# Kernel tuning notes

Hardware: AMD Instinct MI355X
Metric: run time of the kernel (lower is better)

The kernel has to match this reference:

```python
import jax, jax.numpy as jnp
import numpy as np

N_HEAD = 8
D_HEAD = 64  # emb_size == d_model // n_head


def _proj(x, w):
    # x: (B, 1, d_model, max_len), w: (n_head*emb_size, 1, 25, 1) -> conv VALID
    y = jax.lax.conv_general_dilated(
        x, w, window_strides=(1, 1), padding='VALID',
        dimension_numbers=('NCHW', 'OIHW', 'NCHW'))  # (B, C, H1, L)
    B, C, H1, L = y.shape
    y = y.reshape(B, C, H1 // N_HEAD, N_HEAD, L).mean(axis=3)  # (B, C, H2, L)
    # view(B, -1, n_head, d_head).transpose(1, 2) -> (B, n_head, S, d_head)
    y = y.reshape(B, -1, N_HEAD, D_HEAD).transpose(0, 2, 1, 3)
    return y


def setup_inputs() -> dict:
    key = jax.random.key(0)
    ks = jax.random.split(key, 7)
    B, d_model, max_len = 8, 512, 16
    C = N_HEAD * D_HEAD  # 512
    return {
        'query': jax.random.normal(ks[0], (B, 1, d_model, max_len), jnp.float32),
        'key':   jax.random.normal(ks[1], (B, 1, d_model, max_len), jnp.float32),
        'value': jax.random.normal(ks[2], (B, 1, d_model, max_len), jnp.float32),
        'wq': jax.random.normal(ks[3], (C, 1, 25, 1), jnp.float32) * 0.1,
        'wk': jax.random.normal(ks[4], (C, 1, 25, 1), jnp.float32) * 0.1,
        'wv': jax.random.normal(ks[5], (C, 1, 25, 1), jnp.float32) * 0.1,
        'w_out': jax.random.normal(ks[6], (1, 1, 1, 1), jnp.float32),
        'b_out': jnp.zeros((1,), jnp.float32),
    }


def reference(query, key, value, wq, wk, wv, w_out, b_out):
    q = _proj(query, wq)   # (B, H, S, Dh)
    k = _proj(key, wk)
    v = _proj(value, wv)
    scale = 1.0 / jnp.sqrt(jnp.asarray(D_HEAD, q.dtype))
    scores = jnp.einsum('bhqd,bhkd->bhqk', q, k) * scale
    attn = jax.nn.softmax(scores, axis=-1)  # dropout is identity in eval
    x = jnp.einsum('bhqk,bhkd->bhqd', attn, v)
    B = x.shape[0]
    x = x.transpose(0, 2, 1, 3).reshape(B, -1, N_HEAD * D_HEAD)  # (B, S, d_model)
    # conv_out: 1x1 Conv2d(1,1) == scalar scale + bias
    x = x * w_out.reshape(()) + b_out.reshape(())
    return x, attn
```

## Files before the change

### kernel.cpp

```cpp
#include <hip/hip_runtime.h>
#include <hip/hip_bf16.h>
#include <cstdint>
#include <cstddef>

#define B_    8
#define H_    8
#define BH_   64
#define S_    976
#define SP_   992
#define D_    64
#define DM_   512
#define L_    16
#define H2_   61
#define KW_   25
#define EFF_  32
#define XOFF  3997696
#define NWB   49152
#define OSTR  68

typedef __attribute__((ext_vector_type(8))) short bf16x8;
typedef __attribute__((ext_vector_type(4))) float f32x4;

__device__ __forceinline__ unsigned short f2bfu(float f) {
    union { float f; unsigned u; } v; v.f = f;
    unsigned u = v.u;
    u += 0x7fffu + ((u >> 16) & 1u);
    return (unsigned short)(u >> 16);
}
__device__ __forceinline__ unsigned packbf(float a, float b) {
    return (unsigned)f2bfu(a) | ((unsigned)f2bfu(b) << 16);
}
__device__ __forceinline__ float bflo(unsigned u) {
    union { unsigned u; float f; } v; v.u = u << 16; return v.f;
}
__device__ __forceinline__ float bfhi(unsigned u) {
    union { unsigned u; float f; } v; v.u = u & 0xffff0000u; return v.f;
}

__global__ __launch_bounds__(256) void wbar_kernel(
    const float* __restrict__ wq, const float* __restrict__ wk,
    const float* __restrict__ wv, float* __restrict__ wbar,
    short* __restrict__ vtws) {
    int idx = blockIdx.x * 256 + threadIdx.x;
    if (idx < NWB) {
        int t  = idx & 31;
        int c  = (idx >> 5) & 511;
        int tz = idx >> 14;
        const float* w = (tz == 0) ? wq : (tz == 1) ? wk : wv;
        int jlo = (t - 24 > 0) ? t - 24 : 0;
        int jhi = (t < 7) ? t : 7;
        float s = 0.f;
        for (int j = jlo; j <= jhi; ++j) s += w[c * KW_ + (t - j)];
        wbar[idx] = s * 0.125f;
    } else {
        int p = idx - NWB;
        int bh = p >> 10;
        int dh = (p >> 4) & 63;
        int s  = S_ + (p & 15);
        vtws[((size_t)bh * D_ + dh) * SP_ + s] = 0;
    }
}

__global__ __launch_bounds__(256) void proj_kernel(
    const float* __restrict__ qin, const float* __restrict__ kin,
    const float* __restrict__ vin, const float* __restrict__ wbar,
    short* __restrict__ qws, short* __restrict__ kws, short* __restrict__ vtws) {
    __shared__ float xl[536 * L_];
    int blk = blockIdx.x;
    int cg  = blk & 15;
    int b   = (blk >> 4) & 7;
    int tz  = blk >> 7;
    const float* x = (tz == 0) ? qin : (tz == 1) ? kin : vin;

    const float4* xb4 = (const float4*)(x + b * DM_ * L_);
    float4* xl4 = (float4*)xl;
    for (int i = threadIdx.x; i < DM_ * L_ / 4; i += 256) xl4[i] = xb4[i];
    for (int i = DM_ * L_ + threadIdx.x; i < 536 * L_; i += 256) xl[i] = 0.f;

    int c_local = threadIdx.x >> 3;
    int plane   = threadIdx.x & 7;
    int c       = cg * 32 + c_local;
    float wreg[EFF_];
    const float4* wb4 = (const float4*)(wbar + ((size_t)tz * DM_ + c) * EFF_);
    #pragma unroll
    for (int i = 0; i < 8; ++i) {
        float4 t4 = wb4[i];
        wreg[4*i+0] = t4.x; wreg[4*i+1] = t4.y;
        wreg[4*i+2] = t4.z; wreg[4*i+3] = t4.w;
    }
    __syncthreads();

    for (int m = 0; m < 32; ++m) {
        int pg  = plane + 8 * m;
        int h2b = pg >> 4;
        int l   = pg & 15;
        float acc[4] = {0.f, 0.f, 0.f, 0.f};
        #pragma unroll
        for (int k = 0; k < 56; ++k) {
            float xv = xl[(h2b * 32 + k) * L_ + l];
            #pragma unroll
            for (int d = 0; d < 4; ++d) {
                int t = k - 8 * d;
                if (t >= 0 && t < EFF_) acc[d] = fmaf(xv, wreg[t], acc[d]);
            }
        }
        #pragma unroll
        for (int d = 0; d < 4; ++d) {
            int h2 = h2b * 4 + d;
            if (h2 < H2_) {
                int f    = c * S_ + h2 * L_ + l;
                int s    = f >> 9;
                int head = (f >> 6) & 7;
                int dh   = f & 63;
                int bh   = b * H_ + head;
                short bv = (short)f2bfu(acc[d]);
                if (tz == 0)      qws[((size_t)bh * S_ + s) * D_ + dh] = bv;
                else if (tz == 1) kws[((size_t)bh * S_ + s) * D_ + dh] = bv;
                else              vtws[((size_t)bh * D_ + dh) * SP_ + s] = bv;
            }
        }
    }
}

__global__ __launch_bounds__(256) void attn_kernel(
    const short* __restrict__ qws, const short* __restrict__ kws,
    const short* __restrict__ vtws, const float* __restrict__ w_out,
    const float* __restrict__ b_out, float* __restrict__ out) {
    __shared__ short plds[4][16 * 40];
    __shared__ float olds[2][16 * OSTR];
    __shared__ float sums[2][2][16];

    int w    = threadIdx.x >> 6;
    int lane = threadIdx.x & 63;
    int l16  = lane & 15;
    int g    = lane >> 4;
    int p    = w >> 1;
    int h    = w & 1;

    int blk = blockIdx.x;
    int xcd = blk & 7;
    int j   = blk >> 3;
    int bh  = xcd + 8 * (j / 31);
    int pr  = j % 31;
    int qt  = pr * 2 + p;
    bool valid = qt < H2_;
    int s0 = qt * 16;

    int t0 = h ? 30 : 0;
    int nt = h ? 31 : 30;

    unsigned pp[31][2];
    float inv = 0.f;

    if (valid) {
        const short* qb = qws + ((size_t)bh * S_ + s0 + l16) * D_ + g * 8;
        bf16x8 q0 = *(const bf16x8*)qb;
        bf16x8 q1 = *(const bf16x8*)(qb + 32);
        const short* kb0 = kws + ((size_t)bh * S_ + t0 * 16 + l16) * D_ + g * 8;

        float sa = 0.f, sb = 0.f, sc_ = 0.f, sd = 0.f;
        #pragma unroll
        for (int ct = 0; ct < 31; ++ct) {
            if (ct < nt) {
                const short* kb = kb0 + (size_t)ct * 16 * D_;
                bf16x8 k0 = *(const bf16x8*)kb;
                bf16x8 k1 = *(const bf16x8*)(kb + 32);
                f32x4 acc = {0.f, 0.f, 0.f, 0.f};
                acc = __builtin_amdgcn_mfma_f32_16x16x32_bf16(k0, q0, acc, 0, 0, 0);
                acc = __builtin_amdgcn_mfma_f32_16x16x32_bf16(k1, q1, acc, 0, 0, 0);
                float e0 = __expf(acc[0] * 0.125f);
                float e1 = __expf(acc[1] * 0.125f);
                float e2 = __expf(acc[2] * 0.125f);
                float e3 = __expf(acc[3] * 0.125f);
                sa += e0; sb += e1; sc_ += e2; sd += e3;
                pp[ct][0] = packbf(e0, e1);
                pp[ct][1] = packbf(e2, e3);
            }
        }
        float sum = (sa + sb) + (sc_ + sd);
        sum += __shfl_xor(sum, 16);
        sum += __shfl_xor(sum, 32);
        if (lane < 16) sums[p][h][l16] = sum;
    }
    __syncthreads();
    if (valid) inv = 1.f / (sums[p][0][l16] + sums[p][1][l16]);

    f32x4 o0 = {0.f,0.f,0.f,0.f}, o1 = {0.f,0.f,0.f,0.f};
    f32x4 o2 = {0.f,0.f,0.f,0.f}, o3 = {0.f,0.f,0.f,0.f};

    if (valid) {
        float* arow = out + XOFF + ((size_t)bh * S_ + s0 + l16) * S_;
        short* pl = &plds[w][0];
        const short* vrow = vtws + ((size_t)bh * D_ + l16) * SP_ + g * 8;

        #pragma unroll
        for (int c = 0; c < 15; ++c) {
            #pragma unroll
            for (int t = 0; t < 2; ++t) {
                int lt = 2 * c + t;
                int gt = t0 + lt;
                unsigned u0 = pp[lt][0], u1 = pp[lt][1];
                f32x4 pv = { bflo(u0) * inv, bfhi(u0) * inv,
                             bflo(u1) * inv, bfhi(u1) * inv };
                __builtin_nontemporal_store(pv, (f32x4*)(arow + gt * 16 + g * 4));
                uint2 upk = {u0, u1};
                *(uint2*)(void*)(pl + l16 * 40 + t * 16 + g * 4) = upk;
            }
            __threadfence_block();
            bf16x8 pa = *(const bf16x8*)(pl + l16 * 40 + g * 8);
            const short* vb = vrow + t0 * 16 + c * 32;
            o0 = __builtin_amdgcn_mfma_f32_16x16x32_bf16(pa, *(const bf16x8*)(vb), o0, 0, 0, 0);
            o1 = __builtin_amdgcn_mfma_f32_16x16x32_bf16(pa, *(const bf16x8*)(vb + 16 * SP_), o1, 0, 0, 0);
            o2 = __builtin_amdgcn_mfma_f32_16x16x32_bf16(pa, *(const bf16x8*)(vb + 32 * SP_), o2, 0, 0, 0);
            o3 = __builtin_amdgcn_mfma_f32_16x16x32_bf16(pa, *(const bf16x8*)(vb + 48 * SP_), o3, 0, 0, 0);
        }

        if (h) {
            unsigned u0 = pp[30][0], u1 = pp[30][1];
            f32x4 pv = { bflo(u0) * inv, bfhi(u0) * inv,
                         bflo(u1) * inv, bfhi(u1) * inv };
            __builtin_nontemporal_store(pv, (f32x4*)(arow + 60 * 16 + g * 4));
            uint2 upk = {u0, u1};
            *(uint2*)(void*)(pl + l16 * 40 + g * 4) = upk;
            uint2 zz = {0u, 0u};
            *(uint2*)(void*)(pl + l16 * 40 + 16 + g * 4) = zz;
            __threadfence_block();
            bf16x8 pa = *(const bf16x8*)(pl + l16 * 40 + g * 8);
            const short* vb = vrow + 960;
            o0 = __builtin_amdgcn_mfma_f32_16x16x32_bf16(pa, *(const bf16x8*)(vb), o0, 0, 0, 0);
            o1 = __builtin_amdgcn_mfma_f32_16x16x32_bf16(pa, *(const bf16x8*)(vb + 16 * SP_), o1, 0, 0, 0);
            o2 = __builtin_amdgcn_mfma_f32_16x16x32_bf16(pa, *(const bf16x8*)(vb + 32 * SP_), o2, 0, 0, 0);
            o3 = __builtin_amdgcn_mfma_f32_16x16x32_bf16(pa, *(const bf16x8*)(vb + 48 * SP_), o3, 0, 0, 0);
        }

        if (!h) {
            float* ob = &olds[p][0];
            #pragma unroll
            for (int i = 0; i < 4; ++i) {
                int q = g * 4 + i;
                ob[q * OSTR +  0 + l16] = o0[i];
                ob[q * OSTR + 16 + l16] = o1[i];
                ob[q * OSTR + 32 + l16] = o2[i];
                ob[q * OSTR + 48 + l16] = o3[i];
            }
        }
    }
    __syncthreads();

    if (valid && h) {
        float wo = w_out[0], bo = b_out[0];
        int b = bh >> 3, hh = bh & 7;
        const float* ob = &olds[p][0];
        #pragma unroll
        for (int i = 0; i < 4; ++i) {
            int q = g * 4 + i;
            float invr = __shfl(inv, q);
            float s1 = invr * wo;
            float* xr = out + ((size_t)b * S_ + s0 + q) * DM_ + hh * D_ + l16;
            xr[0]  = (o0[i] + ob[q * OSTR +  0 + l16]) * s1 + bo;
            xr[16] = (o1[i] + ob[q * OSTR + 16 + l16]) * s1 + bo;
            xr[32] = (o2[i] + ob[q * OSTR + 32 + l16]) * s1 + bo;
            xr[48] = (o3[i] + ob[q * OSTR + 48 + l16]) * s1 + bo;
        }
    }
}

extern "C" void kernel_launch(void* const* d_in, const int* in_sizes, int n_in,
                              void* d_out, int out_size, void* d_ws, size_t ws_size,
                              hipStream_t stream) {
    const float* q   = (const float*)d_in[0];
    const float* k   = (const float*)d_in[1];
    const float* v   = (const float*)d_in[2];
    const float* wq  = (const float*)d_in[3];
    const float* wk  = (const float*)d_in[4];
    const float* wv  = (const float*)d_in[5];
    const float* wo  = (const float*)d_in[6];
    const float* bo  = (const float*)d_in[7];

    char* ws = (char*)d_ws;
    float* wbar = (float*)ws;
    short* qws  = (short*)(ws + 196608);
    short* kws  = qws + (size_t)BH_ * S_ * D_;
    short* vtws = kws + (size_t)BH_ * S_ * D_;

    wbar_kernel<<<448, 256, 0, stream>>>(wq, wk, wv, wbar, vtws);
    proj_kernel<<<384, 256, 0, stream>>>(q, k, v, wbar, qws, kws, vtws);
    attn_kernel<<<BH_ * 31, 256, 0, stream>>>(qws, kws, vtws, wo, bo,
                                              (float*)d_out);
}
```

Baseline: 162.4 us.

## Split each query tile's keys across four waves instead of two

Each block now handles a single 16-row query tile, and its four waves split the 61 key tiles (16/15/15/15) rather than two waves per tile across two tiles. This removes the invalid-wave padding from the old odd tile count, halves the per-wave register array of probabilities, and launches twice as many blocks for more parallelism. In exchange, Q is loaded by four waves and the final reduction sums three LDS partials per output.

New measurement: 159.8 us. About the same (-1.6%).

```diff
diff --git a/kernel.cpp b/kernel.cpp
--- a/kernel.cpp
+++ b/kernel.cpp
@@ -127,74 +127,69 @@
     const short* __restrict__ vtws, const float* __restrict__ w_out,
     const float* __restrict__ b_out, float* __restrict__ out) {
     __shared__ short plds[4][16 * 40];
-    __shared__ float olds[2][16 * OSTR];
-    __shared__ float sums[2][2][16];
+    __shared__ float olds[3][16 * OSTR];
+    __shared__ float sums[4][16];
 
     int w    = threadIdx.x >> 6;
     int lane = threadIdx.x & 63;
     int l16  = lane & 15;
     int g    = lane >> 4;
-    int p    = w >> 1;
-    int h    = w & 1;
 
     int blk = blockIdx.x;
     int xcd = blk & 7;
     int j   = blk >> 3;
-    int bh  = xcd + 8 * (j / 31);
-    int pr  = j % 31;
-    int qt  = pr * 2 + p;
-    bool valid = qt < H2_;
-    int s0 = qt * 16;
-
-    int t0 = h ? 30 : 0;
-    int nt = h ? 31 : 30;
-
-    unsigned pp[31][2];
-    float inv = 0.f;
-
-    if (valid) {
-        const short* qb = qws + ((size_t)bh * S_ + s0 + l16) * D_ + g * 8;
-        bf16x8 q0 = *(const bf16x8*)qb;
-        bf16x8 q1 = *(const bf16x8*)(qb + 32);
-        const short* kb0 = kws + ((size_t)bh * S_ + t0 * 16 + l16) * D_ + g * 8;
-
-        float sa = 0.f, sb = 0.f, sc_ = 0.f, sd = 0.f;
-        #pragma unroll
-        for (int ct = 0; ct < 31; ++ct) {
-            if (ct < nt) {
-                const short* kb = kb0 + (size_t)ct * 16 * D_;
-                bf16x8 k0 = *(const bf16x8*)kb;
-                bf16x8 k1 = *(const bf16x8*)(kb + 32);
-                f32x4 acc = {0.f, 0.f, 0.f, 0.f};
-                acc = __builtin_amdgcn_mfma_f32_16x16x32_bf16(k0, q0, acc, 0, 0, 0);
-                acc = __builtin_amdgcn_mfma_f32_16x16x32_bf16(k1, q1, acc, 0, 0, 0);
-                float e0 = __expf(acc[0] * 0.125f);
-                float e1 = __expf(acc[1] * 0.125f);
-                float e2 = __expf(acc[2] * 0.125f);
-                float e3 = __expf(acc[3] * 0.125f);
-                sa += e0; sb += e1; sc_ += e2; sd += e3;
-                pp[ct][0] = packbf(e0, e1);
-                pp[ct][1] = packbf(e2, e3);
-            }
-        }
-        float sum = (sa + sb) + (sc_ + sd);
-        sum += __shfl_xor(sum, 16);
-        sum += __shfl_xor(sum, 32);
-        if (lane < 16) sums[p][h][l16] = sum;
-    }
+    int bh  = xcd + 8 * (j / H2_);
+    int qt  = j % H2_;
+    int s0  = qt * 16;
+
+    int t0 = (w == 0) ? 0 : 16 + (w - 1) * 15;
+    int nt = (w == 0) ? 16 : 15;
+
+    unsigned pp[16][2];
+
+    const short* qb = qws + ((size_t)bh * S_ + s0 + l16) * D_ + g * 8;
+    bf16x8 q0 = *(const bf16x8*)qb;
+    bf16x8 q1 = *(const bf16x8*)(qb + 32);
+    const short* kb0 = kws + ((size_t)bh * S_ + t0 * 16 + l16) * D_ + g * 8;
+
+    float sa = 0.f, sb = 0.f, sc_ = 0.f, sd = 0.f;
+    #pragma unroll
+    for (int ct = 0; ct < 16; ++ct) {
+        if (ct < nt) {
+            const short* kb = kb0 + (size_t)ct * 16 * D_;
+            bf16x8 k0 = *(const bf16x8*)kb;
+            bf16x8 k1 = *(const bf16x8*)(kb + 32);
+            f32x4 acc = {0.f, 0.f, 0.f, 0.f};
+            acc = __builtin_amdgcn_mfma_f32_16x16x32_bf16(k0, q0, acc, 0, 0, 0);
+            acc = __builtin_amdgcn_mfma_f32_16x16x32_bf16(k1, q1, acc, 0, 0, 0);
+            float e0 = __expf(acc[0] * 0.125f);
+            float e1 = __expf(acc[1] * 0.125f);
+            float e2 = __expf(acc[2] * 0.125f);
+            float e3 = __expf(acc[3] * 0.125f);
+            sa += e0; sb += e1; sc_ += e2; sd += e3;
+            pp[ct][0] = packbf(e0, e1);
+            pp[ct][1] = packbf(e2, e3);
+        }
+    }
+    float sum = (sa + sb) + (sc_ + sd);
+    sum += __shfl_xor(sum, 16);
+    sum += __shfl_xor(sum, 32);
+    if (lane < 16) sums[w][l16] = sum;
     __syncthreads();
-    if (valid) inv = 1.f / (sums[p][0][l16] + sums[p][1][l16]);
+    float inv = 1.f / ((sums[0][l16] + sums[1][l16]) +
+                       (sums[2][l16] + sums[3][l16]));
 
     f32x4 o0 = {0.f,0.f,0.f,0.f}, o1 = {0.f,0.f,0.f,0.f};
     f32x4 o2 = {0.f,0.f,0.f,0.f}, o3 = {0.f,0.f,0.f,0.f};
 
-    if (valid) {
-        float* arow = out + XOFF + ((size_t)bh * S_ + s0 + l16) * S_;
-        short* pl = &plds[w][0];
-        const short* vrow = vtws + ((size_t)bh * D_ + l16) * SP_ + g * 8;
-
-        #pragma unroll
-        for (int c = 0; c < 15; ++c) {
+    float* arow = out + XOFF + ((size_t)bh * S_ + s0 + l16) * S_;
+    short* pl = &plds[w][0];
+    const short* vrow = vtws + ((size_t)bh * D_ + l16) * SP_ + g * 8;
+
+    int nc = (w == 0) ? 8 : 7;
+    #pragma unroll
+    for (int c = 0; c < 8; ++c) {
+        if (c < nc) {
             #pragma unroll
             for (int t = 0; t < 2; ++t) {
                 int lt = 2 * c + t;
@@ -214,53 +209,53 @@
             o2 = __builtin_amdgcn_mfma_f32_16x16x32_bf16(pa, *(const bf16x8*)(vb + 32 * SP_), o2, 0, 0, 0);
             o3 = __builtin_amdgcn_mfma_f32_16x16x32_bf16(pa, *(const bf16x8*)(vb + 48 * SP_), o3, 0, 0, 0);
         }
-
-        if (h) {
-            unsigned u0 = pp[30][0], u1 = pp[30][1];
-            f32x4 pv = { bflo(u0) * inv, bfhi(u0) * inv,
-                         bflo(u1) * inv, bfhi(u1) * inv };
-            __builtin_nontemporal_store(pv, (f32x4*)(arow + 60 * 16 + g * 4));
-            uint2 upk = {u0, u1};
-            *(uint2*)(void*)(pl + l16 * 40 + g * 4) = upk;
-            uint2 zz = {0u, 0u};
-            *(uint2*)(void*)(pl + l16 * 40 + 16 + g * 4) = zz;
-            __threadfence_block();
-            bf16x8 pa = *(const bf16x8*)(pl + l16 * 40 + g * 8);
-            const short* vb = vrow + 960;
-            o0 = __builtin_amdgcn_mfma_f32_16x16x32_bf16(pa, *(const bf16x8*)(vb), o0, 0, 0, 0);
-            o1 = __builtin_amdgcn_mfma_f32_16x16x32_bf16(pa, *(const bf16x8*)(vb + 16 * SP_), o1, 0, 0, 0);
-            o2 = __builtin_amdgcn_mfma_f32_16x16x32_bf16(pa, *(const bf16x8*)(vb + 32 * SP_), o2, 0, 0, 0);
-            o3 = __builtin_amdgcn_mfma_f32_16x16x32_bf16(pa, *(const bf16x8*)(vb + 48 * SP_), o3, 0, 0, 0);
-        }
-
-        if (!h) {
-            float* ob = &olds[p][0];
-            #pragma unroll
-            for (int i = 0; i < 4; ++i) {
-                int q = g * 4 + i;
-                ob[q * OSTR +  0 + l16] = o0[i];
-                ob[q * OSTR + 16 + l16] = o1[i];
-                ob[q * OSTR + 32 + l16] = o2[i];
-                ob[q * OSTR + 48 + l16] = o3[i];
-            }
+    }
+
+    if (w != 0) {
+        unsigned u0 = pp[14][0], u1 = pp[14][1];
+        f32x4 pv = { bflo(u0) * inv, bfhi(u0) * inv,
+                     bflo(u1) * inv, bfhi(u1) * inv };
+        __builtin_nontemporal_store(pv, (f32x4*)(arow + (t0 + 14) * 16 + g * 4));
+        uint2 upk = {u0, u1};
+        *(uint2*)(void*)(pl + l16 * 40 + g * 4) = upk;
+        uint2 zz = {0u, 0u};
+        *(uint2*)(void*)(pl + l16 * 40 + 16 + g * 4) = zz;
+        __threadfence_block();
+        bf16x8 pa = *(const bf16x8*)(pl + l16 * 40 + g * 8);
+        const short* vb = vrow + t0 * 16 + 224;
+        o0 = __builtin_amdgcn_mfma_f32_16x16x32_bf16(pa, *(const bf16x8*)(vb), o0, 0, 0, 0);
+        o1 = __builtin_amdgcn_mfma_f32_16x16x32_bf16(pa, *(const bf16x8*)(vb + 16 * SP_), o1, 0, 0, 0);
+        o2 = __builtin_amdgcn_mfma_f32_16x16x32_bf16(pa, *(const bf16x8*)(vb + 32 * SP_), o2, 0, 0, 0);
+        o3 = __builtin_amdgcn_mfma_f32_16x16x32_bf16(pa, *(const bf16x8*)(vb + 48 * SP_), o3, 0, 0, 0);
+    }
+
+    if (w != 3) {
+        float* ob = &olds[w][0];
+        #pragma unroll
+        for (int i = 0; i < 4; ++i) {
+            int q = g * 4 + i;
+            ob[q * OSTR +  0 + l16] = o0[i];
+            ob[q * OSTR + 16 + l16] = o1[i];
+            ob[q * OSTR + 32 + l16] = o2[i];
+            ob[q * OSTR + 48 + l16] = o3[i];
         }
     }
     __syncthreads();
 
-    if (valid && h) {
+    if (w == 3) {
         float wo = w_out[0], bo = b_out[0];
         int b = bh >> 3, hh = bh & 7;
-        const float* ob = &olds[p][0];
         #pragma unroll
         for (int i = 0; i < 4; ++i) {
             int q = g * 4 + i;
             float invr = __shfl(inv, q);
             float s1 = invr * wo;
             float* xr = out + ((size_t)b * S_ + s0 + q) * DM_ + hh * D_ + l16;
-            xr[0]  = (o0[i] + ob[q * OSTR +  0 + l16]) * s1 + bo;
-            xr[16] = (o1[i] + ob[q * OSTR + 16 + l16]) * s1 + bo;
-            xr[32] = (o2[i] + ob[q * OSTR + 32 + l16]) * s1 + bo;
-            xr[48] = (o3[i] + ob[q * OSTR + 48 + l16]) * s1 + bo;
+            int o = q * OSTR + l16;
+            xr[0]  = (o0[i] + olds[0][o +  0] + olds[1][o +  0] + olds[2][o +  0]) * s1 + bo;
+            xr[16] = (o1[i] + olds[0][o + 16] + olds[1][o + 16] + olds[2][o + 16]) * s1 + bo;
+            xr[32] = (o2[i] + olds[0][o + 32] + olds[1][o + 32] + olds[2][o + 32]) * s1 + bo;
+            xr[48] = (o3[i] + olds[0][o + 48] + olds[1][o + 48] + olds[2][o + 48]) * s1 + bo;
         }
     }
 }
@@ -285,6 +280,6 @@
 
     wbar_kernel<<<448, 256, 0, stream>>>(wq, wk, wv, wbar, vtws);
     proj_kernel<<<384, 256, 0, stream>>>(q, k, v, wbar, qws, kws, vtws);
-    attn_kernel<<<BH_ * 31, 256, 0, stream>>>(qws, kws, vtws, wo, bo,
-                                              (float*)d_out);
-}
+    attn_kernel<<<BH_ * H2_, 256, 0, stream>>>(qws, kws, vtws, wo, bo,
+                                               (float*)d_out);
+}
```
